# Kernel optimization log

Hardware: AMD Instinct MI355X
Metric: run time of the kernel (lower is better)

Reference implementation:

```python
import jax, jax.numpy as jnp
import numpy as np

HEADS = 8
IH, IW = 32, 32
C_IN, C_OUT = 512, 512


def setup_inputs() -> dict:
    key = jax.random.key(0)
    k1, k2, k3, k4, k5 = jax.random.split(key, 5)
    B = 32
    n = IH + IW + (IH // 2) * (IW // 2)  # pooled kv length = 320
    x = jax.random.normal(k1, (B, C_IN, IH, IW), dtype=jnp.float32)
    # 1x1 conv weights stored as [out, in] (bias-free qkv, biased output proj)
    Wqkv = jax.random.normal(k2, (3 * C_IN, C_IN), dtype=jnp.float32) * 0.02
    Wout = jax.random.normal(k3, (C_OUT, C_IN), dtype=jnp.float32) * 0.02
    bout = jnp.zeros((C_OUT,), dtype=jnp.float32)
    pos_embed = jax.random.normal(k4, (1, IH * IW, n), dtype=jnp.float32) * 0.2
    return {"x": x, "Wqkv": Wqkv, "Wout": Wout, "bout": bout, "pos_embed": pos_embed}


def _pool_gate(t, B, C, H, W):
    # adaptive_avg_pool2d(.,(None,1)) == mean over width -> [B,C,H]
    th = t.mean(axis=3)
    # adaptive_avg_pool2d(.,(1,None)) (+permute) == mean over height -> [B,C,W]
    tw = t.mean(axis=2)
    # adaptive_avg_pool2d to (H//2, W//2) with even dims == 2x2 average pooling
    tp = t.reshape(B, C, H // 2, 2, W // 2, 2).mean(axis=(3, 5)).reshape(B, C, -1)
    s = jax.nn.sigmoid(jnp.concatenate([th, tw, tp], axis=2))  # [B,C,n]
    d = C // HEADS
    # 'b (h d) n -> b h n d'
    return s.reshape(B, HEADS, d, -1).transpose(0, 1, 3, 2)


def reference(x, Wqkv, Wout, bout, pos_embed):
    B, C, H, W = x.shape
    d = C // HEADS
    scale = d ** (-0.5)
    qkv = jnp.einsum('bchw,oc->bohw', x, Wqkv)  # 1x1 conv, no bias
    q, k, v = jnp.split(qkv, 3, axis=1)
    # 'b (h d) ih iw -> b h (ih iw) d'
    q = q.reshape(B, HEADS, d, H * W).transpose(0, 1, 3, 2)
    k = _pool_gate(k, B, C, H, W)  # [B,h,n,d]
    v = _pool_gate(v, B, C, H, W)  # [B,h,n,d]
    dots = jnp.einsum('bhsd,bhnd->bhsn', q, k) * scale + pos_embed  # pos_embed [1,s,n] broadcasts
    attn = jax.nn.softmax(dots, axis=-1)
    out = jnp.einsum('bhsn,bhnd->bhsd', attn, v)
    # 'b h (ih iw) d -> b (h d) ih iw'
    out = out.transpose(0, 1, 3, 2).reshape(B, HEADS * d, H, W)
    out = jnp.einsum('bchw,oc->bohw', out, Wout) + bout[None, :, None, None]
    return out
```

## Files before the change

### kernel.cpp

```cpp
#include <hip/hip_runtime.h>
#include <hip/hip_bf16.h>
#include <math.h>

#define HEADS 8
#define CH    512
#define S     1024
#define NKV   320
#define DH    64
#define BATCH 32

typedef __attribute__((ext_vector_type(8))) short short8;
typedef __attribute__((ext_vector_type(4))) short short4v;
typedef __attribute__((ext_vector_type(4))) float float4v;
typedef __attribute__((ext_vector_type(4))) unsigned int uint4v;

__device__ __forceinline__ short f2bf(float f) {
    __hip_bfloat16 h = __float2bfloat16(f);
    return *reinterpret_cast<short*>(&h);
}

__device__ __forceinline__ float fexp2(float x) {
#if __has_builtin(__builtin_amdgcn_exp2f)
    return __builtin_amdgcn_exp2f(x);
#else
    return exp2f(x);
#endif
}

#define GLOAD_LDS16(gp, lp) __builtin_amdgcn_global_load_lds( \
    (const __attribute__((address_space(1))) void*)(gp),      \
    (__attribute__((address_space(3))) void*)(lp), 16, 0, 0)

__global__ __launch_bounds__(256) void pool_kernel2(const float* __restrict__ x,
                                                    short* __restrict__ xpT) {
    __shared__ float sm[4][1024];
    __shared__ short smT[320 * 34];
    const int w = threadIdx.x >> 6;
    const int l = threadIdx.x & 63;
    const int b = blockIdx.y, c0 = blockIdx.x * 32;
    for (int it = 0; it < 8; ++it) {
        const int cix = it * 4 + w;
        const float* src = x + ((size_t)b * 512 + c0 + cix) * 1024;
        #pragma unroll
        for (int j = 0; j < 16; ++j) sm[w][j * 64 + l] = src[j * 64 + l];
        const float* pl = sm[w];
        #pragma unroll
        for (int g = 0; g < 5; ++g) {
            const int nn = g * 64 + l;
            float r;
            if (nn < 32) {
                const int h = nn; float s = 0.f;
                #pragma unroll
                for (int ww = 0; ww < 32; ++ww) s += pl[h * 32 + ww];
                r = s * (1.0f / 32.0f);
            } else if (nn < 64) {
                const int ww = nn - 32; float s = 0.f;
                #pragma unroll
                for (int h = 0; h < 32; ++h) s += pl[h * 32 + ww];
                r = s * (1.0f / 32.0f);
            } else {
                const int i = nn - 64;
                const int ph = i >> 4, pw = i & 15;
                r = 0.25f * (pl[(2 * ph) * 32 + 2 * pw]     + pl[(2 * ph) * 32 + 2 * pw + 1] +
                             pl[(2 * ph + 1) * 32 + 2 * pw] + pl[(2 * ph + 1) * 32 + 2 * pw + 1]);
            }
            smT[nn * 34 + cix] = f2bf(r);
        }
    }
    __syncthreads();
    short* dst = xpT + (size_t)b * NKV * 512 + c0;
    const int r0 = threadIdx.x >> 4, dwi = threadIdx.x & 15;
    #pragma unroll
    for (int pass = 0; pass < 20; ++pass) {
        const int r = pass * 16 + r0;
        const unsigned int v =
            (unsigned int)(unsigned short)smT[r * 34 + dwi * 2] |
            ((unsigned int)(unsigned short)smT[r * 34 + dwi * 2 + 1] << 16);
        *(unsigned int*)&dst[(size_t)r * 512 + dwi * 2] = v;
    }
}

__global__ __launch_bounds__(256) void tcast(const float* __restrict__ in,
                                             short* __restrict__ out, int R, int C) {
    __shared__ float sm[64][65];
    const int t = threadIdx.x;
    const int c0 = blockIdx.x * 64, r0 = blockIdx.y * 64;
    const float* ib = in + ((size_t)blockIdx.z * R + r0) * C + c0;
    #pragma unroll
    for (int rep = 0; rep < 4; ++rep) {
        const int r = rep * 16 + (t >> 4), c = (t & 15) * 4;
        const float4 v = *(const float4*)&ib[(size_t)r * C + c];
        sm[r][c] = v.x; sm[r][c + 1] = v.y; sm[r][c + 2] = v.z; sm[r][c + 3] = v.w;
    }
    __syncthreads();
    short* ob = out + ((size_t)blockIdx.z * C + c0) * R + r0;
    #pragma unroll
    for (int rep = 0; rep < 4; ++rep) {
        const int cr = rep * 16 + (t >> 4), rc = (t & 15) * 4;
        short4v p;
        #pragma unroll
        for (int e = 0; e < 4; ++e) p[e] = f2bf(sm[rc + e][cr]);
        *(short4v*)&ob[(size_t)cr * R + rc] = p;
    }
}

__global__ __launch_bounds__(256) void castw2(const float* __restrict__ a,
                                              short* __restrict__ oa, int na, int nscale,
                                              const float* __restrict__ b,
                                              short* __restrict__ ob, int nb) {
    const int i = (blockIdx.x * 256 + threadIdx.x) * 4;
    if (i < na) {
        const float sc = (i < nscale) ? 1.4426950408889634f : 1.0f;
        const float4 v = *(const float4*)&a[i];
        short4v p = {f2bf(v.x * sc), f2bf(v.y * sc), f2bf(v.z * sc), f2bf(v.w * sc)};
        *(short4v*)&oa[i] = p;
    } else if (i - na < nb) {
        const int j = i - na;
        const float4 v = *(const float4*)&b[j];
        short4v p = {f2bf(v.x), f2bf(v.y), f2bf(v.z), f2bf(v.w)};
        *(short4v*)&ob[j] = p;
    }
}

template <int MT, int NT, int ACT, typename OT>
__device__ __forceinline__ void gemm_body(short* __restrict__ smem,
                                          int bxs, int bys, int bz,
                                          const short* __restrict__ A, long sAb,
                                          const short* __restrict__ B, long sBb,
                                          const float* __restrict__ bias,
                                          OT* __restrict__ C, int M, int N) {
    constexpr int K  = 512;
    constexpr int BM = 32 * MT, BN = 32 * NT;
    short* As = smem;
    short* Bs = smem + 2 * BM * 64;
    const int t = threadIdx.x, w = t >> 6, l = t & 63;
    const int wm = w >> 1, wn = w & 1, quad = l >> 4, m15 = l & 15;
    const int n0 = bxs * BN, m0 = bys * BM;
    const short* gA = A + (size_t)sAb * bz + (size_t)m0 * K;
    const short* gB = B + (size_t)sBb * bz + (size_t)n0 * K;
    const int lrow = l >> 3;
    const int pc   = l & 7;

    const float4v zf = {0.f, 0.f, 0.f, 0.f};
    float4v acc[MT][NT];
    #pragma unroll
    for (int i = 0; i < MT; ++i)
        #pragma unroll
        for (int j = 0; j < NT; ++j) acc[i][j] = zf;

    auto STAGE = [&](int bf, int k0) {
        #pragma unroll
        for (int ii = w; ii < BM / 8; ii += 4) {
            const int row = ii * 8 + lrow;
            const int x = pc ^ (row & 7);
            GLOAD_LDS16(gA + (size_t)row * K + k0 + x * 8, &As[bf * BM * 64 + ii * 512]);
        }
        #pragma unroll
        for (int ii = w; ii < BN / 8; ii += 4) {
            const int row = ii * 8 + lrow;
            const int x = pc ^ (row & 7);
            GLOAD_LDS16(gB + (size_t)row * K + k0 + x * 8, &Bs[bf * BN * 64 + ii * 512]);
        }
    };

    STAGE(0, 0);
    __syncthreads();
    for (int ks8 = 0; ks8 < 8; ++ks8) {
        const int cur = ks8 & 1;
        if (ks8 < 7) STAGE(cur ^ 1, (ks8 + 1) * 64);
        #pragma unroll
        for (int ks = 0; ks < 2; ++ks) {
            const int xa = (((ks * 4 + quad) ^ (m15 & 7))) * 8;
            short8 aF[MT], bF[NT];
            #pragma unroll
            for (int i = 0; i < MT; ++i)
                aF[i] = *(const short8*)&As[cur * BM * 64 + ((wm * MT + i) * 16 + m15) * 64 + xa];
            #pragma unroll
            for (int j = 0; j < NT; ++j)
                bF[j] = *(const short8*)&Bs[cur * BN * 64 + ((wn * NT + j) * 16 + m15) * 64 + xa];
            #pragma unroll
            for (int i = 0; i < MT; ++i)
                #pragma unroll
                for (int j = 0; j < NT; ++j)
                    acc[i][j] = __builtin_amdgcn_mfma_f32_16x16x32_bf16(aF[i], bF[j], acc[i][j], 0, 0, 0);
        }
        if (ks8 < 7) __syncthreads();
    }

    OT* gC = C + (size_t)bz * M * N;
    #pragma unroll
    for (int i = 0; i < MT; ++i) {
        #pragma unroll
        for (int r = 0; r < 4; ++r) {
            const int row = m0 + (wm * MT + i) * 16 + quad * 4 + r;
            float bv = 0.f;
            if (ACT == 2) bv = bias[row];
            #pragma unroll
            for (int j = 0; j < NT; ++j) {
                const int col = n0 + (wn * NT + j) * 16 + m15;
                float v = acc[i][j][r];
                if (ACT == 1) { v = 1.0f / (1.0f + __expf(-v)); if (col < 512) v *= 0.125f; }
                if (ACT == 2) v += bv;
                if constexpr (sizeof(OT) == 2)
                    ((short*)gC)[(size_t)row * N + col] = f2bf(v);
                else
                    ((float*)gC)[(size_t)row * N + col] = v;
            }
        }
    }
}

__global__ __launch_bounds__(256) void gemm_qkv(const short* __restrict__ xT,
                                                const short* __restrict__ Wq,
                                                const short* __restrict__ xpT,
                                                const short* __restrict__ Wkv,
                                                short* __restrict__ qT,
                                                short* __restrict__ kvT) {
    __shared__ short smem[40960];
    constexpr int T = 1664;
    int lin = blockIdx.x;
    lin = (lin & 7) * (T >> 3) + (lin >> 3);
    if (lin < 1024) {
        const int bxs = lin & 3, bys = (lin >> 2) & 7, bz = lin >> 5;
        gemm_body<4, 4, 0, short>(smem, bxs, bys, bz,
                                  xT, (long)S * CH, Wq, 0, nullptr, qT, S, CH);
    } else {
        const int l2 = lin - 1024;
        const int bxs = l2 & 3, bys = (l2 >> 2) % 5, bz = l2 / 20;
        gemm_body<2, 8, 1, short>(smem, bxs, bys, bz,
                                  xpT, (long)NKV * CH, Wkv, 0, nullptr, kvT, NKV, 2 * CH);
    }
}

template <int MT, int NT, int ACT, typename OT>
__global__ __launch_bounds__(256) void gemm_bf16(const short* __restrict__ A, long sAb,
                                                 const short* __restrict__ B, long sBb,
                                                 const float* __restrict__ bias,
                                                 OT* __restrict__ C, int M, int N) {
    constexpr int BM = 32 * MT, BN = 32 * NT;
    __shared__ short smem[2 * (BM + BN) * 64];
    const int gx = gridDim.x, gy = gridDim.y;
    const int T = gx * gy * gridDim.z;
    int lin = ((int)blockIdx.z * gy + (int)blockIdx.y) * gx + (int)blockIdx.x;
    lin = (lin & 7) * (T >> 3) + (lin >> 3);
    const int bxs = lin % gx;
    const int bys = (lin / gx) % gy;
    const int bz  = lin / (gx * gy);
    gemm_body<MT, NT, ACT, OT>(smem, bxs, bys, bz, A, sAb, B, sBb, bias, C, M, N);
}

__global__ __launch_bounds__(512, 4) void attn_mfma(const short* __restrict__ qT,
                                                    const short* __restrict__ kvT,
                                                    const float* __restrict__ pos,
                                                    short* __restrict__ aoT) {
    __shared__ short smK[8 * 320 * 8];
    __shared__ short smV[64 * 320];
    const int tid = threadIdx.x, w = tid >> 6, l = tid & 63;
    const int quad = l >> 4, m15 = l & 15;
    const int b = blockIdx.z, h = blockIdx.y, s0 = blockIdx.x * 512;
    const short* kvb = kvT + (size_t)b * NKV * 1024;
    constexpr float LOG2E = 1.4426950408889634f;

    const int nperm = (l & 35) | ((l & 12) << 1) | ((l & 16) >> 2);
    #pragma unroll
    for (int i2 = w; i2 < 40; i2 += 8) {
        const int nb = i2 % 5, dg = i2 / 5;
        GLOAD_LDS16(kvb + (size_t)(nb * 64 + nperm) * 1024 + h * 64 + dg * 8,
                    &smK[(dg * 320 + nb * 64) * 8]);
    }
    #pragma unroll
    for (int it = 0; it < 5; ++it) {
        const int i2 = it * 512 + tid;
        const int n5 = i2 & 31, d8 = (i2 >> 5) & 7, nb = i2 >> 8;
        const int n = nb * 32 + n5;
        const short8 v = *(const short8*)&kvb[(size_t)n * 1024 + 512 + h * 64 + d8 * 8];
        const int x = n >> 3;
        #pragma unroll
        for (int e = 0; e < 8; ++e)
            smV[(d8 * 8 + e) * 320 + ((x ^ e) * 8) + (n & 7)] = v[e];
    }

    __syncthreads();

    const short* qbase = qT + (size_t)(b * S + s0 + w * 16 + m15) * 512 + h * 64;
    const float4v zf = {0.f, 0.f, 0.f, 0.f};

    #pragma unroll 1
    for (int sp = 0; sp < 2; ++sp) {
        asm volatile("" ::: "memory");

        const short* qbA = qbase + (size_t)(2 * sp) * 128 * 512;
        const short* qbB = qbA + (size_t)128 * 512;
        const short8 cqA0 = *(const short8*)&qbA[quad * 8];
        const short8 cqA1 = *(const short8*)&qbA[32 + quad * 8];
        const short8 cqB0 = *(const short8*)&qbB[quad * 8];
        const short8 cqB1 = *(const short8*)&qbB[32 + quad * 8];
        const float* posA = pos + (size_t)(s0 + 2 * sp * 128 + w * 16 + m15) * NKV + quad * 8;
        const float* posB = posA + (size_t)128 * NKV;

        float4v OA0 = zf, OA1 = zf, OA2 = zf, OA3 = zf;
        float4v OB0 = zf, OB1 = zf, OB2 = zf, OB3 = zf;
        float lpA = 0.f, lpB = 0.f;

        #pragma unroll
        for (int c = 0; c < 5; ++c) {
            unsigned int PcA[8], PcB[8];
            #pragma unroll
            for (int t4 = 0; t4 < 4; ++t4) {
                const int tt = c * 4 + t4;
                const short8 k0 = *(const short8*)&smK[(quad * 320 + tt * 16 + m15) * 8];
                const short8 k1 = *(const short8*)&smK[((4 + quad) * 320 + tt * 16 + m15) * 8];
                float4v aA = zf, aB = zf;
                aA = __builtin_amdgcn_mfma_f32_16x16x32_bf16(k0, cqA0, aA, 0, 0, 0);
                aA = __builtin_amdgcn_mfma_f32_16x16x32_bf16(k1, cqA1, aA, 0, 0, 0);
                aB = __builtin_amdgcn_mfma_f32_16x16x32_bf16(k0, cqB0, aB, 0, 0, 0);
                aB = __builtin_amdgcn_mfma_f32_16x16x32_bf16(k1, cqB1, aB, 0, 0, 0);
                const int n0 = c * 64 + (t4 >> 1) * 32 + (t4 & 1) * 4;
                const float4 pvA = *(const float4*)&posA[n0];
                const float4 pvB = *(const float4*)&posB[n0];
                const float a0 = fexp2(fmaf(pvA.x, LOG2E, aA[0]));
                const float a1 = fexp2(fmaf(pvA.y, LOG2E, aA[1]));
                const float a2 = fexp2(fmaf(pvA.z, LOG2E, aA[2]));
                const float a3 = fexp2(fmaf(pvA.w, LOG2E, aA[3]));
                const float b0 = fexp2(fmaf(pvB.x, LOG2E, aB[0]));
                const float b1 = fexp2(fmaf(pvB.y, LOG2E, aB[1]));
                const float b2 = fexp2(fmaf(pvB.z, LOG2E, aB[2]));
                const float b3 = fexp2(fmaf(pvB.w, LOG2E, aB[3]));
                lpA += (a0 + a1) + (a2 + a3);
                lpB += (b0 + b1) + (b2 + b3);
                PcA[t4 * 2]     = (unsigned int)(unsigned short)f2bf(a0) |
                                  ((unsigned int)(unsigned short)f2bf(a1) << 16);
                PcA[t4 * 2 + 1] = (unsigned int)(unsigned short)f2bf(a2) |
                                  ((unsigned int)(unsigned short)f2bf(a3) << 16);
                PcB[t4 * 2]     = (unsigned int)(unsigned short)f2bf(b0) |
                                  ((unsigned int)(unsigned short)f2bf(b1) << 16);
                PcB[t4 * 2 + 1] = (unsigned int)(unsigned short)f2bf(b2) |
                                  ((unsigned int)(unsigned short)f2bf(b3) << 16);
            }
            const uint4v uA0 = {PcA[0], PcA[1], PcA[2], PcA[3]};
            const uint4v uA1 = {PcA[4], PcA[5], PcA[6], PcA[7]};
            const uint4v uB0 = {PcB[0], PcB[1], PcB[2], PcB[3]};
            const uint4v uB1 = {PcB[4], PcB[5], PcB[6], PcB[7]};
            const short8 aPA0 = __builtin_bit_cast(short8, uA0);
            const short8 aPA1 = __builtin_bit_cast(short8, uA1);
            const short8 aPB0 = __builtin_bit_cast(short8, uB0);
            const short8 aPB1 = __builtin_bit_cast(short8, uB1);
            #pragma unroll
            for (int ks = 0; ks < 2; ++ks) {
                const short8 aPA = ks ? aPA1 : aPA0;
                const short8 aPB = ks ? aPB1 : aPB0;
                const int xr = (c * 8 + ks * 4 + quad) ^ (m15 & 7);
                const short8 bV0 = *(const short8*)&smV[(0 * 16 + m15) * 320 + xr * 8];
                const short8 bV1 = *(const short8*)&smV[(1 * 16 + m15) * 320 + xr * 8];
                const short8 bV2 = *(const short8*)&smV[(2 * 16 + m15) * 320 + xr * 8];
                const short8 bV3 = *(const short8*)&smV[(3 * 16 + m15) * 320 + xr * 8];
                OA0 = __builtin_amdgcn_mfma_f32_16x16x32_bf16(aPA, bV0, OA0, 0, 0, 0);
                OB0 = __builtin_amdgcn_mfma_f32_16x16x32_bf16(aPB, bV0, OB0, 0, 0, 0);
                OA1 = __builtin_amdgcn_mfma_f32_16x16x32_bf16(aPA, bV1, OA1, 0, 0, 0);
                OB1 = __builtin_amdgcn_mfma_f32_16x16x32_bf16(aPB, bV1, OB1, 0, 0, 0);
                OA2 = __builtin_amdgcn_mfma_f32_16x16x32_bf16(aPA, bV2, OA2, 0, 0, 0);
                OB2 = __builtin_amdgcn_mfma_f32_16x16x32_bf16(aPB, bV2, OB2, 0, 0, 0);
                OA3 = __builtin_amdgcn_mfma_f32_16x16x32_bf16(aPA, bV3, OA3, 0, 0, 0);
                OB3 = __builtin_amdgcn_mfma_f32_16x16x32_bf16(aPB, bV3, OB3, 0, 0, 0);
            }
        }

        float lrA = lpA, lrB = lpB;
        lrA += __shfl_xor(lrA, 16, 64);
        lrA += __shfl_xor(lrA, 32, 64);
        lrB += __shfl_xor(lrB, 16, 64);
        lrB += __shfl_xor(lrB, 32, 64);
        const float invlA = 1.0f / lrA;
        const float invlB = 1.0f / lrB;
        float invA[4], invB[4];
        #pragma unroll
        for (int r = 0; r < 4; ++r) {
            invA[r] = __shfl(invlA, (l & 48) | (quad * 4 + r), 64);
            invB[r] = __shfl(invlB, (l & 48) | (quad * 4 + r), 64);
        }

        #pragma unroll
        for (int r = 0; r < 4; ++r) {
            const int sA = s0 + 2 * sp * 128 + w * 16 + quad * 4 + r;
            short* orA = &aoT[(size_t)(b * S + sA) * 512 + h * 64 + m15];
            orA[0]  = f2bf(OA0[r] * invA[r]);
            orA[16] = f2bf(OA1[r] * invA[r]);
            orA[32] = f2bf(OA2[r] * invA[r]);
            orA[48] = f2bf(OA3[r] * invA[r]);
            short* orB = orA + (size_t)128 * 512;
            orB[0]  = f2bf(OB0[r] * invB[r]);
            orB[16] = f2bf(OB1[r] * invB[r]);
            orB[32] = f2bf(OB2[r] * invB[r]);
            orB[48] = f2bf(OB3[r] * invB[r]);
        }
    }
}

extern "C" void kernel_launch(void* const* d_in, const int* in_sizes, int n_in,
                              void* d_out, int out_size, void* d_ws, size_t ws_size,
                              hipStream_t stream) {
    const float* x    = (const float*)d_in[0];
    const float* Wqkv = (const float*)d_in[1];
    const float* Wout = (const float*)d_in[2];
    const float* bout = (const float*)d_in[3];
    const float* pos  = (const float*)d_in[4];
    char* ws = (char*)d_ws;
    short* xT   = (short*)(ws + 20971520);
    short* xpT  = (short*)(ws + 54525952);
    short* qT   = (short*)(ws + 65011712);
    short* kvT  = (short*)(ws + 98566144);
    short* aoT  = (short*)(ws + 119537664);
    short* Wbf  = (short*)(ws + 153092096);
    short* Wobf = (short*)(ws + 154664960);
    float* out  = (float*)d_out;

    castw2<<<dim3(1024), 256, 0, stream>>>(Wqkv, Wbf, 1536 * 512, 512 * 512,
                                           Wout, Wobf, 512 * 512);
    pool_kernel2<<<dim3(16, BATCH), 256, 0, stream>>>(x, xpT);
    tcast<<<dim3(16, 8, BATCH), 256, 0, stream>>>(x, xT, CH, S);
    gemm_qkv<<<dim3(1664), 256, 0, stream>>>(xT, Wbf, xpT, Wbf + CH * CH, qT, kvT);
    attn_mfma<<<dim3(2, HEADS, BATCH), 512, 0, stream>>>(qT, kvT, pos, aoT);
    gemm_bf16<4, 4, 2, float><<<dim3(8, 4, BATCH), 256, 0, stream>>>(
        Wobf, 0, aoT, (long)S * CH, bout, out, CH, S);
}
```

Measured before the change: 266.6 us.

## Fuse pooling into transpose-cast kernel with atomic width-mean accumulation

```diff
diff --git a/kernel.cpp b/kernel.cpp
--- a/kernel.cpp
+++ b/kernel.cpp
@@ -31,84 +31,91 @@
     (const __attribute__((address_space(1))) void*)(gp),      \
     (__attribute__((address_space(3))) void*)(lp), 16, 0, 0)
 
-__global__ __launch_bounds__(256) void pool_kernel2(const float* __restrict__ x,
-                                                    short* __restrict__ xpT) {
-    __shared__ float sm[4][1024];
-    __shared__ short smT[320 * 34];
-    const int w = threadIdx.x >> 6;
-    const int l = threadIdx.x & 63;
-    const int b = blockIdx.y, c0 = blockIdx.x * 32;
-    for (int it = 0; it < 8; ++it) {
-        const int cix = it * 4 + w;
-        const float* src = x + ((size_t)b * 512 + c0 + cix) * 1024;
-        #pragma unroll
-        for (int j = 0; j < 16; ++j) sm[w][j * 64 + l] = src[j * 64 + l];
-        const float* pl = sm[w];
-        #pragma unroll
-        for (int g = 0; g < 5; ++g) {
-            const int nn = g * 64 + l;
-            float r;
-            if (nn < 32) {
-                const int h = nn; float s = 0.f;
-                #pragma unroll
-                for (int ww = 0; ww < 32; ++ww) s += pl[h * 32 + ww];
-                r = s * (1.0f / 32.0f);
-            } else if (nn < 64) {
-                const int ww = nn - 32; float s = 0.f;
-                #pragma unroll
-                for (int h = 0; h < 32; ++h) s += pl[h * 32 + ww];
-                r = s * (1.0f / 32.0f);
-            } else {
-                const int i = nn - 64;
-                const int ph = i >> 4, pw = i & 15;
-                r = 0.25f * (pl[(2 * ph) * 32 + 2 * pw]     + pl[(2 * ph) * 32 + 2 * pw + 1] +
-                             pl[(2 * ph + 1) * 32 + 2 * pw] + pl[(2 * ph + 1) * 32 + 2 * pw + 1]);
-            }
-            smT[nn * 34 + cix] = f2bf(r);
-        }
-    }
-    __syncthreads();
-    short* dst = xpT + (size_t)b * NKV * 512 + c0;
-    const int r0 = threadIdx.x >> 4, dwi = threadIdx.x & 15;
-    #pragma unroll
-    for (int pass = 0; pass < 20; ++pass) {
-        const int r = pass * 16 + r0;
-        const unsigned int v =
-            (unsigned int)(unsigned short)smT[r * 34 + dwi * 2] |
-            ((unsigned int)(unsigned short)smT[r * 34 + dwi * 2 + 1] << 16);
-        *(unsigned int*)&dst[(size_t)r * 512 + dwi * 2] = v;
-    }
-}
-
-__global__ __launch_bounds__(256) void tcast(const float* __restrict__ in,
-                                             short* __restrict__ out, int R, int C) {
+__global__ __launch_bounds__(256) void tcast2(const float* __restrict__ x,
+                                              short* __restrict__ xT,
+                                              short* __restrict__ xpT,
+                                              float* __restrict__ twbuf) {
     __shared__ float sm[64][65];
     const int t = threadIdx.x;
-    const int c0 = blockIdx.x * 64, r0 = blockIdx.y * 64;
-    const float* ib = in + ((size_t)blockIdx.z * R + r0) * C + c0;
+    const int s0 = blockIdx.x * 64, ch0 = blockIdx.y * 64, b = blockIdx.z;
+    const int hp = blockIdx.x;
+    const float* ib = x + ((size_t)b * 512 + ch0) * 1024 + s0;
     #pragma unroll
     for (int rep = 0; rep < 4; ++rep) {
         const int r = rep * 16 + (t >> 4), c = (t & 15) * 4;
-        const float4 v = *(const float4*)&ib[(size_t)r * C + c];
+        const float4 v = *(const float4*)&ib[(size_t)r * 1024 + c];
         sm[r][c] = v.x; sm[r][c + 1] = v.y; sm[r][c + 2] = v.z; sm[r][c + 3] = v.w;
     }
     __syncthreads();
-    short* ob = out + ((size_t)blockIdx.z * C + c0) * R + r0;
+    short* ob = xT + ((size_t)b * 1024 + s0) * 512 + ch0;
     #pragma unroll
     for (int rep = 0; rep < 4; ++rep) {
-        const int cr = rep * 16 + (t >> 4), rc = (t & 15) * 4;
+        const int sr = rep * 16 + (t >> 4), cc = (t & 15) * 4;
         short4v p;
         #pragma unroll
-        for (int e = 0; e < 4; ++e) p[e] = f2bf(sm[rc + e][cr]);
-        *(short4v*)&ob[(size_t)cr * R + rc] = p;
+        for (int e = 0; e < 4; ++e) p[e] = f2bf(sm[cc + e][sr]);
+        *(short4v*)&ob[(size_t)sr * 512 + cc] = p;
+    }
+    if (t < 128) {
+        const int r = t >> 1, half = t & 1;
+        float s = 0.f;
+        #pragma unroll
+        for (int i = 0; i < 32; ++i) s += sm[r][half * 32 + i];
+        xpT[((size_t)b * NKV + 2 * hp + half) * 512 + ch0 + r] = f2bf(s * (1.0f / 32.0f));
+    }
+    {
+        const int r = t >> 2, pwq = (t & 3) * 4;
+        #pragma unroll
+        for (int k = 0; k < 4; ++k) {
+            const int pw = pwq + k;
+            const float v = 0.25f * (sm[r][2 * pw] + sm[r][2 * pw + 1] +
+                                     sm[r][32 + 2 * pw] + sm[r][32 + 2 * pw + 1]);
+            xpT[((size_t)b * NKV + 64 + hp * 16 + pw) * 512 + ch0 + r] = f2bf(v);
+        }
+    }
+    {
+        const int w = t & 31, rb = (t >> 5) * 8;
+        #pragma unroll
+        for (int k = 0; k < 8; ++k) {
+            const int r = rb + k;
+            atomicAdd(&twbuf[((size_t)b * 512 + ch0 + r) * 32 + w],
+                      sm[r][w] + sm[r][32 + w]);
+        }
+    }
+}
+
+__global__ __launch_bounds__(256) void twfin(const float* __restrict__ twbuf,
+                                             short* __restrict__ xpT) {
+    __shared__ short lds[32 * 514];
+    const int b = blockIdx.x, t = threadIdx.x;
+    #pragma unroll
+    for (int i = 0; i < 64; ++i) {
+        const int j = i * 256 + t;
+        const int c = j >> 5, w = j & 31;
+        lds[w * 514 + c] = f2bf(twbuf[(size_t)b * 16384 + j] * (1.0f / 32.0f));
+    }
+    __syncthreads();
+    short* dst = xpT + ((size_t)b * NKV + 32) * 512;
+    #pragma unroll
+    for (int rr = 0; rr < 32; ++rr) {
+        const unsigned int v =
+            (unsigned int)(unsigned short)lds[rr * 514 + t * 2] |
+            ((unsigned int)(unsigned short)lds[rr * 514 + t * 2 + 1] << 16);
+        *(unsigned int*)&dst[(size_t)rr * 512 + t * 2] = v;
     }
 }
 
 __global__ __launch_bounds__(256) void castw2(const float* __restrict__ a,
                                               short* __restrict__ oa, int na, int nscale,
                                               const float* __restrict__ b,
-                                              short* __restrict__ ob, int nb) {
-    const int i = (blockIdx.x * 256 + threadIdx.x) * 4;
+                                              short* __restrict__ ob, int nb,
+                                              float* __restrict__ twbuf) {
+    const int gid = blockIdx.x * 256 + threadIdx.x;
+    const int i = gid * 4;
+    if (gid < 131072) {
+        const float4 z = {0.f, 0.f, 0.f, 0.f};
+        ((float4*)twbuf)[gid] = z;
+    }
     if (i < na) {
         const float sc = (i < nscale) ? 1.4426950408889634f : 1.0f;
         const float4 v = *(const float4*)&a[i];
@@ -405,6 +412,7 @@
     const float* bout = (const float*)d_in[3];
     const float* pos  = (const float*)d_in[4];
     char* ws = (char*)d_ws;
+    float* twbuf = (float*)(ws + 0);
     short* xT   = (short*)(ws + 20971520);
     short* xpT  = (short*)(ws + 54525952);
     short* qT   = (short*)(ws + 65011712);
@@ -415,9 +423,9 @@
     float* out  = (float*)d_out;
 
     castw2<<<dim3(1024), 256, 0, stream>>>(Wqkv, Wbf, 1536 * 512, 512 * 512,
-                                           Wout, Wobf, 512 * 512);
-    pool_kernel2<<<dim3(16, BATCH), 256, 0, stream>>>(x, xpT);
-    tcast<<<dim3(16, 8, BATCH), 256, 0, stream>>>(x, xT, CH, S);
+                                           Wout, Wobf, 512 * 512, twbuf);
+    tcast2<<<dim3(16, 8, BATCH), 256, 0, stream>>>(x, xT, xpT, twbuf);
+    twfin<<<dim3(BATCH), 256, 0, stream>>>(twbuf, xpT);
     gemm_qkv<<<dim3(1664), 256, 0, stream>>>(xT, Wbf, xpT, Wbf + CH * CH, qT, kvT);
     attn_mfma<<<dim3(2, HEADS, BATCH), 512, 0, stream>>>(qT, kvT, pos, aoT);
     gemm_bf16<4, 4, 2, float><<<dim3(8, 4, BATCH), 256, 0, stream>>>(
```

Result: no change. 271.9 us (+2.0%).
